# Kernel optimization log

Hardware: AMD Instinct MI355X
Metric: run time of the kernel (lower is better)

## Reference

```python
import jax, jax.numpy as jnp
import numpy as np

N_EMBD = 768
FULL_SIZE = 16 * N_EMBD   # 12288
K = 4 * N_EMBD            # iter_size = 3072 (top-k)
B, T = 8, 1024


def setup_inputs() -> dict:
    key = jax.random.key(0)
    k0, k1, k2, k3, k4 = jax.random.split(key, 5)
    s = lambda fan_in: 1.0 / np.sqrt(fan_in)
    return {
        "x": jax.random.normal(k0, (B, T, N_EMBD), dtype=jnp.float32),
        "w1": jax.random.normal(k1, (N_EMBD // 16, N_EMBD), dtype=jnp.float32) * s(N_EMBD),
        "w2": jax.random.normal(k2, (FULL_SIZE, N_EMBD // 16), dtype=jnp.float32) * s(N_EMBD // 16),
        "w_mfc": jax.random.normal(k3, (FULL_SIZE, N_EMBD), dtype=jnp.float32) * s(N_EMBD),
        "w_proj": jax.random.normal(k4, (N_EMBD, FULL_SIZE), dtype=jnp.float32) * s(FULL_SIZE),
    }


def _topk_mask(ck, k):
    # softmax -> top-k indices -> hard 0/1 mask (scatter of constant 1.0)
    probs = jax.nn.softmax(ck, axis=-1)
    _, idx = jax.lax.top_k(probs, k)            # (B, k)
    b = jnp.arange(probs.shape[0])[:, None]
    return jnp.zeros_like(probs).at[b, idx].set(1.0)


def reference(x, w1, w2, w_mfc, w_proj):
    # control net on sequence-mean pooled features
    pooled = x.mean(axis=1)                                  # (B, D)
    ck = jax.nn.relu(pooled @ w1.T) @ w2.T                   # (B, F)
    mask = _topk_mask(ck, K)                                 # (B, F) hard 0/1
    # DynamicMaskedLinear: bmm(x, (W*mask)^T) == (x @ W^T) * mask (0/1 output mask)
    h = jnp.einsum('btd,fd->btf', x, w_mfc) * mask[:, None, :]
    h = jax.nn.relu(h)
    out = jnp.einsum('btf,ef->bte', h, w_proj)               # (B, T, D)
    return out
```

## Files before the change

### kernel.cpp

```cpp
#include <hip/hip_runtime.h>

#define N_EMBD 768
#define FULL   12288
#define KSEL   3072
#define BATCH  8
#define TLEN   1024
#define HID    48

typedef short bf16x8 __attribute__((ext_vector_type(8)));
typedef float f32x4 __attribute__((ext_vector_type(4)));
typedef unsigned short u16x4 __attribute__((ext_vector_type(4)));
typedef unsigned short u16x8 __attribute__((ext_vector_type(8)));

#define MFMA(a, b, c) __builtin_amdgcn_mfma_f32_16x16x32_bf16((a), (b), (c), 0, 0, 0)
#define GLDS(g, l) __builtin_amdgcn_global_load_lds( \
    (const __attribute__((address_space(1))) void*)(const void*)(g), \
    (__attribute__((address_space(3))) void*)(void*)(l), 16, 0, 0)

__device__ __forceinline__ unsigned short f2bf(float f) {
  unsigned u = __float_as_uint(f);
  u += 0x7fffu + ((u >> 16) & 1u);
  return (unsigned short)(u >> 16);
}
__device__ __forceinline__ float bf2f(unsigned short h) {
  return __uint_as_float(((unsigned)h) << 16);
}

__global__ void split_pool_x(const float* __restrict__ x, unsigned short* __restrict__ xh,
                             unsigned short* __restrict__ xl, float* __restrict__ partial) {
  const int s = blockIdx.x;
  const int b = blockIdx.y;
  const int d = blockIdx.z * 256 + threadIdx.x * 4;
  const float* base = x + ((size_t)(b * TLEN + s * 64)) * N_EMBD + d;
  float4 sum = {0.f, 0.f, 0.f, 0.f};
  for (int t = 0; t < 64; ++t) {
    const float4 v = *(const float4*)(base + (size_t)t * N_EMBD);
    sum.x += v.x; sum.y += v.y; sum.z += v.z; sum.w += v.w;
    u16x4 h, l;
    h.x = f2bf(v.x); l.x = f2bf(v.x - bf2f(h.x));
    h.y = f2bf(v.y); l.y = f2bf(v.y - bf2f(h.y));
    h.z = f2bf(v.z); l.z = f2bf(v.z - bf2f(h.z));
    h.w = f2bf(v.w); l.w = f2bf(v.w - bf2f(h.w));
    const size_t o = ((size_t)(b * TLEN + s * 64 + t)) * N_EMBD + d;
    *(u16x4*)(xh + o) = h;
    *(u16x4*)(xl + o) = l;
  }
  float* pp = partial + (b * 16 + s) * N_EMBD + d;
  pp[0] = sum.x; pp[1] = sum.y; pp[2] = sum.z; pp[3] = sum.w;
}

__global__ void pool_final_kernel(const float* __restrict__ partial, float* __restrict__ pooled) {
  const int b = blockIdx.x;
  const int tid = threadIdx.x;
  for (int d = tid; d < N_EMBD; d += 256) {
    float sum = 0.f;
    #pragma unroll
    for (int s = 0; s < 16; ++s) sum += partial[(b * 16 + s) * N_EMBD + d];
    pooled[b * N_EMBD + d] = sum * (1.f / TLEN);
  }
}

__global__ __launch_bounds__(256) void control1_kernel(
    const float* __restrict__ pooled, const float* __restrict__ w1, float* __restrict__ hid) {
  __shared__ float w1s[HID][385];
  __shared__ float ps[N_EMBD];
  const int b = blockIdx.x;
  const int tid = threadIdx.x;
  for (int d = tid; d < N_EMBD; d += 256) ps[d] = pooled[b * N_EMBD + d];
  float acc = 0.f;
  #pragma unroll
  for (int half = 0; half < 2; ++half) {
    __syncthreads();
    for (int i = tid; i < HID * 384; i += 256) {
      const int r = i / 384, c = i % 384;
      w1s[r][c] = w1[r * N_EMBD + half * 384 + c];
    }
    __syncthreads();
    if (tid < HID) {
      const float* pr = ps + half * 384;
      #pragma unroll 8
      for (int d2 = 0; d2 < 384; ++d2) acc = fmaf(pr[d2], w1s[tid][d2], acc);
    }
  }
  if (tid < HID) hid[b * HID + tid] = fmaxf(acc, 0.f);
}

__global__ void control2_kernel(const float* __restrict__ hid, const float* __restrict__ w2,
                                float* __restrict__ ck) {
  const int b = blockIdx.y;
  const int f = blockIdx.x * 256 + threadIdx.x;
  __shared__ float hid_s[HID];
  if (threadIdx.x < HID) hid_s[threadIdx.x] = hid[b * HID + threadIdx.x];
  __syncthreads();
  const float* wr = w2 + (size_t)f * HID;
  float acc = 0.f;
  #pragma unroll
  for (int j = 0; j < HID; ++j) acc = fmaf(hid_s[j], wr[j], acc);
  ck[b * FULL + f] = acc;
}

__global__ void topk_kernel(const float* __restrict__ ck, int* __restrict__ sel) {
  const int b = blockIdx.x;
  const int tid = threadIdx.x;
  const int lane = tid & 63, wv = tid >> 6;
  unsigned key[48];
  const int f_lo = tid * 48;
  #pragma unroll
  for (int i = 0; i < 48; ++i) {
    unsigned u = __float_as_uint(ck[b * FULL + f_lo + i]);
    key[i] = (u & 0x80000000u) ? ~u : (u | 0x80000000u);
  }
  __shared__ unsigned redw[4];
  __shared__ int sg[257], se[257];
  unsigned prefix = 0;
  int remaining = KSEL;
  for (int bit = 31; bit >= 0; --bit) {
    const unsigned want = prefix | (1u << bit);
    const unsigned shifted = want >> bit;
    int cnt = 0;
    #pragma unroll
    for (int i = 0; i < 48; ++i) cnt += ((key[i] >> bit) == shifted) ? 1 : 0;
    #pragma unroll
    for (int off = 1; off < 64; off <<= 1) cnt += __shfl_xor(cnt, off, 64);
    if (lane == 0) redw[wv] = (unsigned)cnt;
    __syncthreads();
    const int c = (int)(redw[0] + redw[1] + redw[2] + redw[3]);
    __syncthreads();
    if (c >= remaining) prefix = want;
    else remaining -= c;
  }
  const unsigned kth = prefix;
  int cg = 0, ce = 0;
  #pragma unroll
  for (int i = 0; i < 48; ++i) { cg += (key[i] > kth) ? 1 : 0; ce += (key[i] == kth) ? 1 : 0; }
  sg[tid] = cg; se[tid] = ce;
  __syncthreads();
  if (tid == 0) {
    int ag = 0, ae = 0;
    for (int i = 0; i < 256; ++i) {
      int tg = sg[i], te = se[i];
      sg[i] = ag; se[i] = ae;
      ag += tg; ae += te;
    }
    sg[256] = ag;
  }
  __syncthreads();
  const int ng = sg[256];
  int gpos = sg[tid], epos = se[tid];
  #pragma unroll
  for (int i = 0; i < 48; ++i) {
    const unsigned k = key[i];
    const int f = f_lo + i;
    if (k > kth) {
      sel[b * KSEL + (gpos++)] = f;
    } else if (k == kth) {
      const int p = ng + epos;
      if (p < KSEL) sel[b * KSEL + p] = f;
      ++epos;
    }
  }
}

__global__ void round_w_kernel(const float* __restrict__ src, unsigned short* __restrict__ dst, int n4) {
  const int idx = blockIdx.x * 256 + threadIdx.x;
  if (idx >= n4) return;
  const float4 v = ((const float4*)src)[idx];
  u16x4 h;
  h.x = f2bf(v.x); h.y = f2bf(v.y); h.z = f2bf(v.z); h.w = f2bf(v.w);
  ((u16x4*)dst)[idx] = h;
}

__global__ __launch_bounds__(256) void gather_wp_kernel(
    const float* __restrict__ wproj, const int* __restrict__ sel,
    unsigned short* __restrict__ wph) {
  __shared__ int sel_s[KSEL];
  const int eg = blockIdx.x;
  const int b  = blockIdx.y;
  const int tid = threadIdx.x;
  for (int i = tid; i < KSEL; i += 256) sel_s[i] = sel[b * KSEL + i];
  __syncthreads();
  for (int e = eg * 16; e < eg * 16 + 16; ++e) {
    const float* wr = wproj + (size_t)e * FULL;
    unsigned short* orow = wph + ((size_t)(b * N_EMBD + e)) * KSEL;
    for (int c = tid; c < KSEL / 8; c += 256) {
      const int k0 = c * 8;
      u16x8 v;
      #pragma unroll
      for (int j = 0; j < 8; ++j) v[j] = f2bf(wr[sel_s[k0 + j]]);
      *(u16x8*)(orow + k0) = v;
    }
  }
}

__global__ __launch_bounds__(256) void gemm1_mfma(
    const unsigned short* __restrict__ xh, const unsigned short* __restrict__ xl,
    const unsigned short* __restrict__ wh, const int* __restrict__ sel,
    unsigned short* __restrict__ hh) {
  __shared__ __align__(16) char sm[49152];
  const int nx = TLEN / 128, ny = KSEL / 128;
  const int nwg = nx * ny * BATCH;
  int lin = blockIdx.x + nx * (blockIdx.y + ny * blockIdx.z);
  int swz = (lin & 7) * (nwg >> 3) + (lin >> 3);
  const int bx = swz % nx; int tmp = swz / nx;
  const int by = tmp % ny; const int b = tmp / ny;
  const int t0 = bx * 128, f0 = by * 128;

  const int tid = threadIdx.x;
  const int wv = tid >> 6, lane = tid & 63;
  const int srow = tid >> 2, sslot = tid & 3;
  const int wb = wv * 1024;

  const char* pxh = (const char*)xh;
  const char* pxl = (const char*)xl;
  const char* pwh = (const char*)wh;
  const size_t aoff  = ((size_t)(b * TLEN + t0 + srow)) * 1536 + sslot * 16;
  const size_t aoff2 = aoff + (size_t)64 * 1536;
  const int* selb = sel + b * KSEL;
  const size_t boff  = (size_t)selb[f0 + srow] * 1536 + sslot * 16;
  const size_t boff2 = (size_t)selb[f0 + srow + 64] * 1536 + sslot * 16;

  const int fr = lane & 15, kg = lane >> 4;
  const int fo = fr * 64 + kg * 16;
  const int m0 = (wv >> 1) * 64, n0 = (wv & 1) * 64;

  f32x4 acc[4][4];
  const f32x4 z4 = {0.f, 0.f, 0.f, 0.f};
  #pragma unroll
  for (int mi = 0; mi < 4; ++mi)
    #pragma unroll
    for (int ni = 0; ni < 4; ++ni) acc[mi][ni] = z4;

  auto stage = [&](int bo, int d) {
    GLDS(pxh + aoff  + d, sm + bo + 0     + wb);
    GLDS(pxh + aoff2 + d, sm + bo + 4096  + wb);
    GLDS(pxl + aoff  + d, sm + bo + 8192  + wb);
    GLDS(pxl + aoff2 + d, sm + bo + 12288 + wb);
    GLDS(pwh + boff  + d, sm + bo + 16384 + wb);
    GLDS(pwh + boff2 + d, sm + bo + 20480 + wb);
  };
  stage(0, 0);
  __syncthreads();
  const int NIT = N_EMBD * 2 / 64;
  for (int it = 0; it < NIT; ++it) {
    const int cur = (it & 1) ? 24576 : 0;
    if (it + 1 < NIT) stage(cur ^ 24576, (it + 1) * 64);
    bf16x8 ah[4], al[4], bh[4];
    #pragma unroll
    for (int i = 0; i < 4; ++i) {
      const int ra = (m0 + i * 16) * 64 + fo;
      const int rb = (n0 + i * 16) * 64 + fo;
      ah[i] = *(const bf16x8*)(sm + cur + 0     + ra);
      al[i] = *(const bf16x8*)(sm + cur + 8192  + ra);
      bh[i] = *(const bf16x8*)(sm + cur + 16384 + rb);
    }
    #pragma unroll
    for (int mi = 0; mi < 4; ++mi)
      #pragma unroll
      for (int ni = 0; ni < 4; ++ni) {
        acc[mi][ni] = MFMA(ah[mi], bh[ni], acc[mi][ni]);
        acc[mi][ni] = MFMA(al[mi], bh[ni], acc[mi][ni]);
      }
    __syncthreads();
  }
  unsigned short* lh = (unsigned short*)sm;
  const int rowg = lane >> 4, colc = lane & 15;
  #pragma unroll
  for (int mi = 0; mi < 4; ++mi)
    #pragma unroll
    for (int ni = 0; ni < 4; ++ni) {
      const int row = m0 + mi * 16 + rowg * 4;
      const int col = n0 + ni * 16 + colc;
      #pragma unroll
      for (int j = 0; j < 4; ++j)
        lh[(row + j) * 128 + col] = f2bf(fmaxf(acc[mi][ni][j], 0.f));
    }
  __syncthreads();
  const int orow = tid >> 4, oc = tid & 15;
  #pragma unroll
  for (int i2 = 0; i2 < 8; ++i2) {
    const int row = orow + i2 * 16;
    const u16x8 v = *(const u16x8*)&lh[row * 128 + oc * 8];
    *(u16x8*)(hh + ((size_t)(b * TLEN + t0 + row)) * KSEL + f0 + oc * 8) = v;
  }
}

__global__ __launch_bounds__(256) void gemm2_mfma(
    const unsigned short* __restrict__ hh, const unsigned short* __restrict__ wph,
    float* __restrict__ out) {
  __shared__ __align__(16) char sm[49152];
  const int nx = TLEN / 128, ny = N_EMBD / 64;
  const int nwg = nx * ny * BATCH;
  int lin = blockIdx.x + nx * (blockIdx.y + ny * blockIdx.z);
  int swz = (lin & 7) * (nwg >> 3) + (lin >> 3);
  const int bx = swz % nx; int tmp = swz / nx;
  const int by = tmp % ny; const int b = tmp / ny;
  const int t0 = bx * 128, e0 = by * 64;

  const int tid = threadIdx.x;
  const int wv = tid >> 6, lane = tid & 63;
  const int wb = wv * 1024;

  const char* pa = (const char*)hh;
  const char* pb = (const char*)wph;
  const size_t aoff  = ((size_t)(b * TLEN + t0 + (tid >> 2))) * 6144 + (tid & 3) * 16;
  const size_t aoff2 = aoff + (size_t)64 * 6144;
  const size_t boff  = ((size_t)(b * N_EMBD + e0 + (tid >> 2))) * 6144 + (tid & 3) * 16;

  const int fr = lane & 15, kg = lane >> 4;
  const int fo = fr * 64 + kg * 16;
  const int m0 = (wv >> 1) * 64, n0 = (wv & 1) * 32;

  f32x4 acc[4][2];
  const f32x4 z4 = {0.f, 0.f, 0.f, 0.f};
  #pragma unroll
  for (int mi = 0; mi < 4; ++mi)
    #pragma unroll
    for (int ni = 0; ni < 2; ++ni) acc[mi][ni] = z4;

  auto stage = [&](int bo, int d) {
    GLDS(pa + aoff  + d,      sm + bo + 0     + wb);
    GLDS(pa + aoff2 + d,      sm + bo + 4096  + wb);
    GLDS(pa + aoff  + d + 64, sm + bo + 8192  + wb);
    GLDS(pa + aoff2 + d + 64, sm + bo + 12288 + wb);
    GLDS(pb + boff  + d,      sm + bo + 16384 + wb);
    GLDS(pb + boff  + d + 64, sm + bo + 20480 + wb);
  };
  stage(0, 0);
  __syncthreads();
  const int NIT = KSEL * 2 / 128;
  for (int it = 0; it < NIT; ++it) {
    const int cur = (it & 1) ? 24576 : 0;
    if (it + 1 < NIT) stage(cur ^ 24576, (it + 1) * 128);
    bf16x8 ah[4][2], bh[2][2];
    #pragma unroll
    for (int i = 0; i < 4; ++i) {
      const int ra = (m0 + i * 16) * 64 + fo;
      ah[i][0] = *(const bf16x8*)(sm + cur + 0    + ra);
      ah[i][1] = *(const bf16x8*)(sm + cur + 8192 + ra);
    }
    #pragma unroll
    for (int i = 0; i < 2; ++i) {
      const int rb = (n0 + i * 16) * 64 + fo;
      bh[i][0] = *(const bf16x8*)(sm + cur + 16384 + rb);
      bh[i][1] = *(const bf16x8*)(sm + cur + 20480 + rb);
    }
    #pragma unroll
    for (int c = 0; c < 2; ++c)
      #pragma unroll
      for (int mi = 0; mi < 4; ++mi)
        #pragma unroll
        for (int ni = 0; ni < 2; ++ni)
          acc[mi][ni] = MFMA(ah[mi][c], bh[ni][c], acc[mi][ni]);
    __syncthreads();
  }
  const int rowg = lane >> 4, colc = lane & 15;
  #pragma unroll
  for (int mi = 0; mi < 4; ++mi)
    #pragma unroll
    for (int ni = 0; ni < 2; ++ni) {
      const int m = t0 + m0 + mi * 16 + rowg * 4;
      const int e = e0 + n0 + ni * 16 + colc;
      const size_t base = ((size_t)(b * TLEN + m)) * N_EMBD + e;
      #pragma unroll
      for (int j = 0; j < 4; ++j)
        out[base + (size_t)j * N_EMBD] = acc[mi][ni][j];
    }
}

extern "C" void kernel_launch(void* const* d_in, const int* in_sizes, int n_in,
                              void* d_out, int out_size, void* d_ws, size_t ws_size,
                              hipStream_t stream) {
  const float* x      = (const float*)d_in[0];
  const float* w1     = (const float*)d_in[1];
  const float* w2     = (const float*)d_in[2];
  const float* w_mfc  = (const float*)d_in[3];
  const float* w_proj = (const float*)d_in[4];
  float* out = (float*)d_out;

  char* ws = (char*)d_ws;
  size_t off = 0;
  auto alloc = [&](size_t bytes) -> void* {
    void* p = ws + off;
    off += (bytes + 255) & ~(size_t)255;
    return p;
  };
  const size_t NX  = (size_t)BATCH * TLEN * N_EMBD;
  const size_t NW  = (size_t)FULL * N_EMBD;
  const size_t NWP = (size_t)BATCH * N_EMBD * KSEL;
  const size_t NH  = (size_t)BATCH * TLEN * KSEL;

  float* partial = (float*)alloc((size_t)BATCH * 16 * N_EMBD * 4);
  float* pooled  = (float*)alloc((size_t)BATCH * N_EMBD * 4);
  float* hid     = (float*)alloc((size_t)BATCH * HID * 4);
  float* ckbuf   = (float*)alloc((size_t)BATCH * FULL * 4);
  int*   sel     = (int*)  alloc((size_t)BATCH * KSEL * 4);
  unsigned short* xh  = (unsigned short*)alloc(NX * 2);
  unsigned short* xl  = (unsigned short*)alloc(NX * 2);
  unsigned short* wh  = (unsigned short*)alloc(NW * 2);
  unsigned short* wph = (unsigned short*)alloc(NWP * 2);
  unsigned short* hh  = (unsigned short*)alloc(NH * 2);

  split_pool_x<<<dim3(16, BATCH, 3), 64, 0, stream>>>(x, xh, xl, partial);
  round_w_kernel<<<(int)(NW / 4 / 256), 256, 0, stream>>>(w_mfc, wh, (int)(NW / 4));
  pool_final_kernel<<<BATCH, 256, 0, stream>>>(partial, pooled);
  control1_kernel<<<BATCH, 256, 0, stream>>>(pooled, w1, hid);
  control2_kernel<<<dim3(FULL / 256, BATCH), 256, 0, stream>>>(hid, w2, ckbuf);
  topk_kernel<<<BATCH, 256, 0, stream>>>(ckbuf, sel);
  gather_wp_kernel<<<dim3(48, BATCH), 256, 0, stream>>>(w_proj, sel, wph);
  gemm1_mfma<<<dim3(TLEN / 128, KSEL / 128, BATCH), 256, 0, stream>>>(xh, xl, wh, sel, hh);
  gemm2_mfma<<<dim3(TLEN / 128, N_EMBD / 64, BATCH), 256, 0, stream>>>(hh, wph, out);
}
```

Measured before the change: 395.4 us.

## Enlarge gemm2 tile, stage w_proj rows in LDS for gather, fuse pooling

gemm2 moves from 128x64 tiles with 128-wide K steps to 128x128 tiles with 64-wide K steps and a 4x4 accumulator per wave. This doubles reuse of each A tile, halves the number of workgroups to 384, and groups blocks by batch. The w_proj gather now loads one full row per block into LDS as bf16 and serves all batches from it, so scattered global reads become LDS lookups. The pool-final kernel is folded into control1, removing one launch. The larger gemm2 tile adds register pressure and leaves fewer workgroups to spread across CUs.

```diff
diff --git a/kernel.cpp b/kernel.cpp
--- a/kernel.cpp
+++ b/kernel.cpp
@@ -49,24 +49,18 @@
   pp[0] = sum.x; pp[1] = sum.y; pp[2] = sum.z; pp[3] = sum.w;
 }
 
-__global__ void pool_final_kernel(const float* __restrict__ partial, float* __restrict__ pooled) {
+__global__ __launch_bounds__(256) void control1_kernel(
+    const float* __restrict__ partial, const float* __restrict__ w1, float* __restrict__ hid) {
+  __shared__ float w1s[HID][385];
+  __shared__ float ps[N_EMBD];
   const int b = blockIdx.x;
   const int tid = threadIdx.x;
   for (int d = tid; d < N_EMBD; d += 256) {
     float sum = 0.f;
     #pragma unroll
     for (int s = 0; s < 16; ++s) sum += partial[(b * 16 + s) * N_EMBD + d];
-    pooled[b * N_EMBD + d] = sum * (1.f / TLEN);
-  }
-}
-
-__global__ __launch_bounds__(256) void control1_kernel(
-    const float* __restrict__ pooled, const float* __restrict__ w1, float* __restrict__ hid) {
-  __shared__ float w1s[HID][385];
-  __shared__ float ps[N_EMBD];
-  const int b = blockIdx.x;
-  const int tid = threadIdx.x;
-  for (int d = tid; d < N_EMBD; d += 256) ps[d] = pooled[b * N_EMBD + d];
+    ps[d] = sum * (1.f / TLEN);
+  }
   float acc = 0.f;
   #pragma unroll
   for (int half = 0; half < 2; ++half) {
@@ -173,22 +167,30 @@
 __global__ __launch_bounds__(256) void gather_wp_kernel(
     const float* __restrict__ wproj, const int* __restrict__ sel,
     unsigned short* __restrict__ wph) {
-  __shared__ int sel_s[KSEL];
-  const int eg = blockIdx.x;
-  const int b  = blockIdx.y;
+  __shared__ unsigned short row_s[FULL];
+  const int e = blockIdx.x;
   const int tid = threadIdx.x;
-  for (int i = tid; i < KSEL; i += 256) sel_s[i] = sel[b * KSEL + i];
-  __syncthreads();
-  for (int e = eg * 16; e < eg * 16 + 16; ++e) {
-    const float* wr = wproj + (size_t)e * FULL;
-    unsigned short* orow = wph + ((size_t)(b * N_EMBD + e)) * KSEL;
-    for (int c = tid; c < KSEL / 8; c += 256) {
-      const int k0 = c * 8;
-      u16x8 v;
-      #pragma unroll
-      for (int j = 0; j < 8; ++j) v[j] = f2bf(wr[sel_s[k0 + j]]);
-      *(u16x8*)(orow + k0) = v;
-    }
+  const float* wr = wproj + (size_t)e * FULL;
+  #pragma unroll
+  for (int i = 0; i < FULL / 4 / 256; ++i) {
+    const int idx = tid + i * 256;
+    const float4 v = ((const float4*)wr)[idx];
+    u16x4 h;
+    h.x = f2bf(v.x); h.y = f2bf(v.y); h.z = f2bf(v.z); h.w = f2bf(v.w);
+    *(u16x4*)(row_s + idx * 4) = h;
+  }
+  __syncthreads();
+  #pragma unroll
+  for (int i = 0; i < 12; ++i) {
+    const int idx = tid + i * 256;
+    const int b = idx / 384, c = idx % 384;
+    const int* sp = sel + b * KSEL + c * 8;
+    const int4 s0 = ((const int4*)sp)[0];
+    const int4 s1 = ((const int4*)sp)[1];
+    u16x8 v;
+    v[0] = row_s[s0.x]; v[1] = row_s[s0.y]; v[2] = row_s[s0.z]; v[3] = row_s[s0.w];
+    v[4] = row_s[s1.x]; v[5] = row_s[s1.y]; v[6] = row_s[s1.z]; v[7] = row_s[s1.w];
+    *(u16x8*)(wph + ((size_t)(b * N_EMBD + e)) * KSEL + c * 8) = v;
   }
 }
 
@@ -287,14 +289,12 @@
 __global__ __launch_bounds__(256) void gemm2_mfma(
     const unsigned short* __restrict__ hh, const unsigned short* __restrict__ wph,
     float* __restrict__ out) {
-  __shared__ __align__(16) char sm[49152];
-  const int nx = TLEN / 128, ny = N_EMBD / 64;
-  const int nwg = nx * ny * BATCH;
-  int lin = blockIdx.x + nx * (blockIdx.y + ny * blockIdx.z);
-  int swz = (lin & 7) * (nwg >> 3) + (lin >> 3);
-  const int bx = swz % nx; int tmp = swz / nx;
-  const int by = tmp % ny; const int b = tmp / ny;
-  const int t0 = bx * 128, e0 = by * 64;
+  __shared__ __align__(16) char sm[32768];
+  const int lin = blockIdx.x;
+  const int b = lin & 7;
+  const int j = lin >> 3;
+  const int bx = j & 7, by = j >> 3;
+  const int t0 = bx * 128, e0 = by * 128;
 
   const int tid = threadIdx.x;
   const int wv = tid >> 6, lane = tid & 63;
@@ -305,65 +305,55 @@
   const size_t aoff  = ((size_t)(b * TLEN + t0 + (tid >> 2))) * 6144 + (tid & 3) * 16;
   const size_t aoff2 = aoff + (size_t)64 * 6144;
   const size_t boff  = ((size_t)(b * N_EMBD + e0 + (tid >> 2))) * 6144 + (tid & 3) * 16;
+  const size_t boff2 = boff + (size_t)64 * 6144;
 
   const int fr = lane & 15, kg = lane >> 4;
   const int fo = fr * 64 + kg * 16;
-  const int m0 = (wv >> 1) * 64, n0 = (wv & 1) * 32;
-
-  f32x4 acc[4][2];
+  const int m0 = (wv >> 1) * 64, n0 = (wv & 1) * 64;
+
+  f32x4 acc[4][4];
   const f32x4 z4 = {0.f, 0.f, 0.f, 0.f};
   #pragma unroll
   for (int mi = 0; mi < 4; ++mi)
     #pragma unroll
-    for (int ni = 0; ni < 2; ++ni) acc[mi][ni] = z4;
+    for (int ni = 0; ni < 4; ++ni) acc[mi][ni] = z4;
 
   auto stage = [&](int bo, int d) {
-    GLDS(pa + aoff  + d,      sm + bo + 0     + wb);
-    GLDS(pa + aoff2 + d,      sm + bo + 4096  + wb);
-    GLDS(pa + aoff  + d + 64, sm + bo + 8192  + wb);
-    GLDS(pa + aoff2 + d + 64, sm + bo + 12288 + wb);
-    GLDS(pb + boff  + d,      sm + bo + 16384 + wb);
-    GLDS(pb + boff  + d + 64, sm + bo + 20480 + wb);
+    GLDS(pa + aoff  + d, sm + bo + 0     + wb);
+    GLDS(pa + aoff2 + d, sm + bo + 4096  + wb);
+    GLDS(pb + boff  + d, sm + bo + 8192  + wb);
+    GLDS(pb + boff2 + d, sm + bo + 12288 + wb);
   };
   stage(0, 0);
   __syncthreads();
-  const int NIT = KSEL * 2 / 128;
+  const int NIT = KSEL * 2 / 64;
   for (int it = 0; it < NIT; ++it) {
-    const int cur = (it & 1) ? 24576 : 0;
-    if (it + 1 < NIT) stage(cur ^ 24576, (it + 1) * 128);
-    bf16x8 ah[4][2], bh[2][2];
+    const int cur = (it & 1) ? 16384 : 0;
+    if (it + 1 < NIT) stage(cur ^ 16384, (it + 1) * 64);
+    bf16x8 ah[4], bh[4];
     #pragma unroll
     for (int i = 0; i < 4; ++i) {
-      const int ra = (m0 + i * 16) * 64 + fo;
-      ah[i][0] = *(const bf16x8*)(sm + cur + 0    + ra);
-      ah[i][1] = *(const bf16x8*)(sm + cur + 8192 + ra);
-    }
-    #pragma unroll
-    for (int i = 0; i < 2; ++i) {
-      const int rb = (n0 + i * 16) * 64 + fo;
-      bh[i][0] = *(const bf16x8*)(sm + cur + 16384 + rb);
-      bh[i][1] = *(const bf16x8*)(sm + cur + 20480 + rb);
-    }
-    #pragma unroll
-    for (int c = 0; c < 2; ++c)
+      ah[i] = *(const bf16x8*)(sm + cur + 0    + (m0 + i * 16) * 64 + fo);
+      bh[i] = *(const bf16x8*)(sm + cur + 8192 + (n0 + i * 16) * 64 + fo);
+    }
+    #pragma unroll
+    for (int mi = 0; mi < 4; ++mi)
       #pragma unroll
-      for (int mi = 0; mi < 4; ++mi)
-        #pragma unroll
-        for (int ni = 0; ni < 2; ++ni)
-          acc[mi][ni] = MFMA(ah[mi][c], bh[ni][c], acc[mi][ni]);
+      for (int ni = 0; ni < 4; ++ni)
+        acc[mi][ni] = MFMA(ah[mi], bh[ni], acc[mi][ni]);
     __syncthreads();
   }
   const int rowg = lane >> 4, colc = lane & 15;
   #pragma unroll
   for (int mi = 0; mi < 4; ++mi)
     #pragma unroll
-    for (int ni = 0; ni < 2; ++ni) {
+    for (int ni = 0; ni < 4; ++ni) {
       const int m = t0 + m0 + mi * 16 + rowg * 4;
       const int e = e0 + n0 + ni * 16 + colc;
       const size_t base = ((size_t)(b * TLEN + m)) * N_EMBD + e;
       #pragma unroll
-      for (int j = 0; j < 4; ++j)
-        out[base + (size_t)j * N_EMBD] = acc[mi][ni][j];
+      for (int jj = 0; jj < 4; ++jj)
+        out[base + (size_t)jj * N_EMBD] = acc[mi][ni][jj];
     }
 }
 
@@ -390,7 +380,6 @@
   const size_t NH  = (size_t)BATCH * TLEN * KSEL;
 
   float* partial = (float*)alloc((size_t)BATCH * 16 * N_EMBD * 4);
-  float* pooled  = (float*)alloc((size_t)BATCH * N_EMBD * 4);
   float* hid     = (float*)alloc((size_t)BATCH * HID * 4);
   float* ckbuf   = (float*)alloc((size_t)BATCH * FULL * 4);
   int*   sel     = (int*)  alloc((size_t)BATCH * KSEL * 4);
@@ -402,11 +391,10 @@
 
   split_pool_x<<<dim3(16, BATCH, 3), 64, 0, stream>>>(x, xh, xl, partial);
   round_w_kernel<<<(int)(NW / 4 / 256), 256, 0, stream>>>(w_mfc, wh, (int)(NW / 4));
-  pool_final_kernel<<<BATCH, 256, 0, stream>>>(partial, pooled);
-  control1_kernel<<<BATCH, 256, 0, stream>>>(pooled, w1, hid);
+  control1_kernel<<<BATCH, 256, 0, stream>>>(partial, w1, hid);
   control2_kernel<<<dim3(FULL / 256, BATCH), 256, 0, stream>>>(hid, w2, ckbuf);
   topk_kernel<<<BATCH, 256, 0, stream>>>(ckbuf, sel);
-  gather_wp_kernel<<<dim3(48, BATCH), 256, 0, stream>>>(w_proj, sel, wph);
+  gather_wp_kernel<<<768, 256, 0, stream>>>(w_proj, sel, wph);
   gemm1_mfma<<<dim3(TLEN / 128, KSEL / 128, BATCH), 256, 0, stream>>>(xh, xl, wh, sel, hh);
-  gemm2_mfma<<<dim3(TLEN / 128, N_EMBD / 64, BATCH), 256, 0, stream>>>(hh, wph, out);
-}
+  gemm2_mfma<<<384, 256, 0, stream>>>(hh, wph, out);
+}
```

After: 382.5 us. -3.3%, faster.
